# Optimization experiments

Hardware: AMD Instinct MI355X
Metric: run time of the kernel (lower is better)

## Reference

```python
import jax, jax.numpy as jnp
import numpy as np

HEAD_DIM = 4  # hard-coded by rosa_4bit_layer's reshape(B, T, -1, 4)


def setup_inputs() -> dict:
    key = jax.random.key(0)
    B, T, C = 4, 4096, 512
    kq, kk, kv = jax.random.split(key, 3)
    xq = jax.random.normal(kq, (B, T, C), dtype=jnp.float32)
    xk = jax.random.normal(kk, (B, T, C), dtype=jnp.float32)
    xv = jax.random.normal(kv, (B, T, C), dtype=jnp.float32)
    emb = jnp.ones((1, 1, C), dtype=jnp.float32)  # nn.Parameter(torch.ones((1,1,C)))
    return {"xq": xq, "xk": xk, "xv": xv, "emb": emb}


def _rosa_sufa(q, k, v):
    # q,k,v: (B, H, T, d) with d = 4.
    # Causal linear-attention recurrence with per-head d x d state:
    #   S_t = S_{t-1} + k_t v_t^T ;  o_t = q_t^T S_t
    # expressed as a cumulative sum over outer products (vectorized over T).
    kv = jnp.cumsum(k[..., :, None] * v[..., None, :], axis=2)  # (B,H,T,d,d)
    return jnp.einsum('bhtd,bhtde->bhte', q, kv)                # (B,H,T,d)


def reference(xq, xk, xv, emb):
    B, T, C = xq.shape
    H = C // HEAD_DIM
    # (B,T,C) -> (B,T,H,4) -> (B,H,T,4)
    q = xq.reshape(B, T, H, HEAD_DIM).transpose(0, 2, 1, 3)
    k = xk.reshape(B, T, H, HEAD_DIM).transpose(0, 2, 1, 3)
    v = xv.reshape(B, T, H, HEAD_DIM).transpose(0, 2, 1, 3)
    o = _rosa_sufa(q, k, v)
    # (B,H,T,4) -> (B,T,C)
    o = o.transpose(0, 2, 1, 3).reshape(B, T, C)
    return o * emb
```

## Files before the change

kernel.cpp:

```cpp
#include <hip/hip_runtime.h>


constexpr int B  = 4;
constexpr int T  = 4096;
constexpr int C  = 512;
constexpr int CT = 16;
constexpr int NC = T / CT;
constexpr int NBLK = B * NC;

__global__ __launch_bounds__(512, 8) void k_partial(const float* __restrict__ k,
                                                    const float* __restrict__ v,
                                                    float* __restrict__ part) {
  const int bc  = blockIdx.x;
  const int b   = bc >> 8;
  const int c   = bc & (NC - 1);
  const int tid = threadIdx.x;
  const int h   = tid >> 2;
  const int e   = tid & 3;
  const int t0  = c * CT;

  const size_t base = ((size_t)b * T + t0) * (size_t)C + (h << 2);
  const float* kb = k + base;
  const float* vb = v + base + e;

  float4 acc = {0.f, 0.f, 0.f, 0.f};
#pragma unroll
  for (int t = 0; t < CT; ++t) {
    const float4 k4 = *reinterpret_cast<const float4*>(kb + (size_t)t * C);
    const float  ve = vb[(size_t)t * C];
    acc.x += k4.x * ve;
    acc.y += k4.y * ve;
    acc.z += k4.z * ve;
    acc.w += k4.w * ve;
  }
  reinterpret_cast<float4*>(part)[(size_t)bc * 512 + tid] = acc;
}

__global__ __launch_bounds__(512, 4) void k_scan(float* __restrict__ part) {
  const int sb = blockIdx.x >> 5;
  const int jt = blockIdx.x & 31;
  const int tid = threadIdx.x;
  const int jl = tid & 63;
  const int ci = tid >> 6;
  const int j  = (jt << 6) + jl;
  float* basep = part + (size_t)sb * NC * 2048 + j;
  const int c0 = ci * 32;

  float vals[32];
#pragma unroll
  for (int i = 0; i < 32; ++i) vals[i] = basep[(size_t)(c0 + i) * 2048];
  float sum = 0.f;
#pragma unroll
  for (int i = 0; i < 32; ++i) sum += vals[i];

  __shared__ float lsum[8][64];
  lsum[ci][jl] = sum;
  __syncthreads();
  float run = 0.f;
#pragma unroll
  for (int g = 0; g < 7; ++g)
    if (g < ci) run += lsum[g][jl];
#pragma unroll
  for (int i = 0; i < 32; ++i) {
    basep[(size_t)(c0 + i) * 2048] = run;
    run += vals[i];
  }
}

__global__ __launch_bounds__(512, 8) void k_out(const float* __restrict__ q,
                                                const float* __restrict__ k,
                                                const float* __restrict__ v,
                                                const float* __restrict__ emb,
                                                const float* __restrict__ part,
                                                float* __restrict__ out) {
  const int bc  = blockIdx.x;
  const int b   = bc >> 8;
  const int c   = bc & (NC - 1);
  const int tid = threadIdx.x;
  const int h   = tid >> 2;
  const int e   = tid & 3;
  const int t0  = c * CT;

  float4 S = reinterpret_cast<const float4*>(part)[(size_t)bc * 512 + tid];

  const size_t base = ((size_t)b * T + t0) * (size_t)C + (h << 2);
  const float* qb = q + base;
  const float* kb = k + base;
  const float* vb = v + base + e;
  float*       ob = out + base + e;
  const float embv = emb[(h << 2) + e];

#pragma unroll
  for (int t = 0; t < CT; ++t) {
    const float4 k4 = *reinterpret_cast<const float4*>(kb + (size_t)t * C);
    const float4 q4 = *reinterpret_cast<const float4*>(qb + (size_t)t * C);
    const float  ve = vb[(size_t)t * C];
    S.x += k4.x * ve;
    S.y += k4.y * ve;
    S.z += k4.z * ve;
    S.w += k4.w * ve;
    const float o = q4.x * S.x + q4.y * S.y + q4.z * S.z + q4.w * S.w;
    ob[(size_t)t * C] = o * embv;
  }
}

extern "C" void kernel_launch(void* const* d_in, const int* in_sizes, int n_in,
                              void* d_out, int out_size, void* d_ws, size_t ws_size,
                              hipStream_t stream) {
  const float* xq  = (const float*)d_in[0];
  const float* xk  = (const float*)d_in[1];
  const float* xv  = (const float*)d_in[2];
  const float* emb = (const float*)d_in[3];
  float* out  = (float*)d_out;
  float* part = (float*)d_ws;

  k_partial<<<NBLK, 512, 0, stream>>>(xk, xv, part);
  k_scan<<<B * 32, 512, 0, stream>>>(part);
  k_out<<<NBLK, 512, 0, stream>>>(xq, xk, xv, emb, part, out);
}
```

Measured before the change: 146.9 us.

## Use per-head full-state threads with larger chunks and in-block sub-chunk scan

Each thread now owns a whole 4x4 head state and loads full float4 rows of k, v and q instead of one scalar v element per thread. Chunks grow from 16 to 32 timesteps and are split into four sub-groups that are combined through shared memory, which halves the number of chunk partials the scan must process. The output kernel computes local sub-chunk results, does an intra-block prefix over sub-groups, then re-reads q to add the carried state and writes float4 outputs. In exchange it adds more registers per thread (lower occupancy bound), a shared-memory sync and a second read of q.

```diff
diff --git a/kernel.cpp b/kernel.cpp
--- a/kernel.cpp
+++ b/kernel.cpp
@@ -1,106 +1,151 @@
 #include <hip/hip_runtime.h>
 
 
-constexpr int B  = 4;
-constexpr int T  = 4096;
-constexpr int C  = 512;
-constexpr int CT = 16;
-constexpr int NC = T / CT;
+constexpr int B   = 4;
+constexpr int T   = 4096;
+constexpr int C   = 512;
+constexpr int H   = 128;
+constexpr int NC  = 128;
+constexpr int CT  = T / NC;
+constexpr int SG  = 4;
+constexpr int TSS = CT / SG;
 constexpr int NBLK = B * NC;
 
-__global__ __launch_bounds__(512, 8) void k_partial(const float* __restrict__ k,
+__device__ __forceinline__ void fmadd4(float4& a, float s, const float4& b) {
+  a.x += s * b.x; a.y += s * b.y; a.z += s * b.z; a.w += s * b.w;
+}
+__device__ __forceinline__ void add4(float4& a, const float4& b) {
+  a.x += b.x; a.y += b.y; a.z += b.z; a.w += b.w;
+}
+
+__global__ __launch_bounds__(512, 4) void k_partial(const float* __restrict__ k,
                                                     const float* __restrict__ v,
-                                                    float* __restrict__ part) {
+                                                    float4* __restrict__ part) {
   const int bc  = blockIdx.x;
-  const int b   = bc >> 8;
+  const int b   = bc >> 7;
   const int c   = bc & (NC - 1);
   const int tid = threadIdx.x;
-  const int h   = tid >> 2;
-  const int e   = tid & 3;
-  const int t0  = c * CT;
+  const int sg  = tid >> 7;
+  const int h   = tid & 127;
+  const int t0  = c * CT + sg * TSS;
 
-  const size_t base = ((size_t)b * T + t0) * (size_t)C + (h << 2);
-  const float* kb = k + base;
-  const float* vb = v + base + e;
+  const size_t rb = ((size_t)b * T + t0) * (size_t)C + h * 4;
+  const float* kp = k + rb;
+  const float* vp = v + rb;
 
-  float4 acc = {0.f, 0.f, 0.f, 0.f};
+  float4 S0{0,0,0,0}, S1{0,0,0,0}, S2{0,0,0,0}, S3{0,0,0,0};
 #pragma unroll
-  for (int t = 0; t < CT; ++t) {
-    const float4 k4 = *reinterpret_cast<const float4*>(kb + (size_t)t * C);
-    const float  ve = vb[(size_t)t * C];
-    acc.x += k4.x * ve;
-    acc.y += k4.y * ve;
-    acc.z += k4.z * ve;
-    acc.w += k4.w * ve;
+  for (int t = 0; t < TSS; ++t) {
+    const float4 k4 = *reinterpret_cast<const float4*>(kp + (size_t)t * C);
+    const float4 v4 = *reinterpret_cast<const float4*>(vp + (size_t)t * C);
+    fmadd4(S0, k4.x, v4); fmadd4(S1, k4.y, v4);
+    fmadd4(S2, k4.z, v4); fmadd4(S3, k4.w, v4);
   }
-  reinterpret_cast<float4*>(part)[(size_t)bc * 512 + tid] = acc;
+
+  __shared__ float4 lds[SG][4][H];
+  lds[sg][0][h] = S0; lds[sg][1][h] = S1;
+  lds[sg][2][h] = S2; lds[sg][3][h] = S3;
+  __syncthreads();
+  if (sg == 0) {
+#pragma unroll
+    for (int g = 1; g < SG; ++g) {
+      add4(S0, lds[g][0][h]); add4(S1, lds[g][1][h]);
+      add4(S2, lds[g][2][h]); add4(S3, lds[g][3][h]);
+    }
+    float4* pr = part + (size_t)bc * 512 + h * 4;
+    pr[0] = S0; pr[1] = S1; pr[2] = S2; pr[3] = S3;
+  }
 }
 
 __global__ __launch_bounds__(512, 4) void k_scan(float* __restrict__ part) {
-  const int sb = blockIdx.x >> 5;
-  const int jt = blockIdx.x & 31;
+  const int sb  = blockIdx.x >> 5;
+  const int jt  = blockIdx.x & 31;
   const int tid = threadIdx.x;
-  const int jl = tid & 63;
-  const int ci = tid >> 6;
-  const int j  = (jt << 6) + jl;
-  float* basep = part + (size_t)sb * NC * 2048 + j;
-  const int c0 = ci * 32;
-
-  float vals[32];
+  const int jl  = tid & 63;
+  const int cg  = tid >> 6;
+  const int j   = jt * 64 + jl;
+  float* bp = part + (size_t)sb * NC * 2048 + j;
+  const int c0 = cg * 16;
+  float vals[16];
 #pragma unroll
-  for (int i = 0; i < 32; ++i) vals[i] = basep[(size_t)(c0 + i) * 2048];
+  for (int i = 0; i < 16; ++i) vals[i] = bp[(size_t)(c0 + i) * 2048];
   float sum = 0.f;
 #pragma unroll
-  for (int i = 0; i < 32; ++i) sum += vals[i];
-
-  __shared__ float lsum[8][64];
-  lsum[ci][jl] = sum;
+  for (int i = 0; i < 16; ++i) sum += vals[i];
+  __shared__ float ls[8][64];
+  ls[cg][jl] = sum;
   __syncthreads();
   float run = 0.f;
 #pragma unroll
   for (int g = 0; g < 7; ++g)
-    if (g < ci) run += lsum[g][jl];
+    if (g < cg) run += ls[g][jl];
 #pragma unroll
-  for (int i = 0; i < 32; ++i) {
-    basep[(size_t)(c0 + i) * 2048] = run;
+  for (int i = 0; i < 16; ++i) {
+    bp[(size_t)(c0 + i) * 2048] = run;
     run += vals[i];
   }
 }
 
-__global__ __launch_bounds__(512, 8) void k_out(const float* __restrict__ q,
+__global__ __launch_bounds__(512, 4) void k_out(const float* __restrict__ q,
                                                 const float* __restrict__ k,
                                                 const float* __restrict__ v,
                                                 const float* __restrict__ emb,
-                                                const float* __restrict__ part,
+                                                const float4* __restrict__ part,
                                                 float* __restrict__ out) {
   const int bc  = blockIdx.x;
-  const int b   = bc >> 8;
+  const int b   = bc >> 7;
   const int c   = bc & (NC - 1);
   const int tid = threadIdx.x;
-  const int h   = tid >> 2;
-  const int e   = tid & 3;
-  const int t0  = c * CT;
+  const int sg  = tid >> 7;
+  const int h   = tid & 127;
+  const int t0  = c * CT + sg * TSS;
 
-  float4 S = reinterpret_cast<const float4*>(part)[(size_t)bc * 512 + tid];
+  const float4* pr = part + (size_t)bc * 512 + h * 4;
+  float4 P0 = pr[0], P1 = pr[1], P2 = pr[2], P3 = pr[3];
 
-  const size_t base = ((size_t)b * T + t0) * (size_t)C + (h << 2);
-  const float* qb = q + base;
-  const float* kb = k + base;
-  const float* vb = v + base + e;
-  float*       ob = out + base + e;
-  const float embv = emb[(h << 2) + e];
+  const size_t rb = ((size_t)b * T + t0) * (size_t)C + h * 4;
+  const float* kp = k + rb;
+  const float* vp = v + rb;
+  const float* qp = q + rb;
 
+  float4 olocal[TSS];
+  float4 A0{0,0,0,0}, A1{0,0,0,0}, A2{0,0,0,0}, A3{0,0,0,0};
 #pragma unroll
-  for (int t = 0; t < CT; ++t) {
-    const float4 k4 = *reinterpret_cast<const float4*>(kb + (size_t)t * C);
-    const float4 q4 = *reinterpret_cast<const float4*>(qb + (size_t)t * C);
-    const float  ve = vb[(size_t)t * C];
-    S.x += k4.x * ve;
-    S.y += k4.y * ve;
-    S.z += k4.z * ve;
-    S.w += k4.w * ve;
-    const float o = q4.x * S.x + q4.y * S.y + q4.z * S.z + q4.w * S.w;
-    ob[(size_t)t * C] = o * embv;
+  for (int t = 0; t < TSS; ++t) {
+    const float4 k4 = *reinterpret_cast<const float4*>(kp + (size_t)t * C);
+    const float4 v4 = *reinterpret_cast<const float4*>(vp + (size_t)t * C);
+    const float4 q4 = *reinterpret_cast<const float4*>(qp + (size_t)t * C);
+    fmadd4(A0, k4.x, v4); fmadd4(A1, k4.y, v4);
+    fmadd4(A2, k4.z, v4); fmadd4(A3, k4.w, v4);
+    float4 o{0.f, 0.f, 0.f, 0.f};
+    fmadd4(o, q4.x, A0); fmadd4(o, q4.y, A1);
+    fmadd4(o, q4.z, A2); fmadd4(o, q4.w, A3);
+    olocal[t] = o;
+  }
+
+  __shared__ float4 lds[SG][4][H];
+  lds[sg][0][h] = A0; lds[sg][1][h] = A1;
+  lds[sg][2][h] = A2; lds[sg][3][h] = A3;
+  __syncthreads();
+  float4 S0 = P0, S1 = P1, S2 = P2, S3 = P3;
+#pragma unroll
+  for (int g = 0; g < SG - 1; ++g) {
+    if (g < sg) {
+      add4(S0, lds[g][0][h]); add4(S1, lds[g][1][h]);
+      add4(S2, lds[g][2][h]); add4(S3, lds[g][3][h]);
+    }
+  }
+
+  const float4 e4 = *reinterpret_cast<const float4*>(emb + h * 4);
+  float* op = out + rb;
+#pragma unroll
+  for (int t = 0; t < TSS; ++t) {
+    const float4 q4 = *reinterpret_cast<const float4*>(qp + (size_t)t * C);
+    float4 o = olocal[t];
+    fmadd4(o, q4.x, S0); fmadd4(o, q4.y, S1);
+    fmadd4(o, q4.z, S2); fmadd4(o, q4.w, S3);
+    o.x *= e4.x; o.y *= e4.y; o.z *= e4.z; o.w *= e4.w;
+    *reinterpret_cast<float4*>(op + (size_t)t * C) = o;
   }
 }
 
@@ -111,10 +156,10 @@
   const float* xk  = (const float*)d_in[1];
   const float* xv  = (const float*)d_in[2];
   const float* emb = (const float*)d_in[3];
-  float* out  = (float*)d_out;
-  float* part = (float*)d_ws;
+  float*  out  = (float*)d_out;
+  float4* part = (float4*)d_ws;
 
   k_partial<<<NBLK, 512, 0, stream>>>(xk, xv, part);
-  k_scan<<<B * 32, 512, 0, stream>>>(part);
+  k_scan<<<B * 32, 512, 0, stream>>>((float*)d_ws);
   k_out<<<NBLK, 512, 0, stream>>>(xq, xk, xv, emb, part, out);
 }
```

New measurement: 175.6 us. 19.5% more time.
